# Performance work log

Hardware: AMD Instinct MI355X
Metric: run time of the kernel (lower is better)

Reference implementation:

```python
import jax, jax.numpy as jnp
import numpy as np

B, C, H, W = 4, 64, 256, 256
HEADS, DHEAD = 4, 64
INNER = HEADS * DHEAD


def setup_inputs() -> dict:
    key = jax.random.key(0)
    ks = jax.random.split(key, 8)
    s = 1.0 / np.sqrt(C)
    return {
        "x_in": jax.random.normal(ks[0], (B, C, H, W), jnp.float32),
        "illu_fea_trans": jax.random.normal(ks[1], (B, C, H, W), jnp.float32),
        "Wq": jax.random.normal(ks[2], (C, INNER), jnp.float32) * s,
        "Wk": jax.random.normal(ks[3], (C, INNER), jnp.float32) * s,
        "Wv": jax.random.normal(ks[4], (C, INNER), jnp.float32) * s,
        "WL": jax.random.normal(ks[5], (C, INNER), jnp.float32) * s,
        "rescale": jnp.ones((HEADS, 1, 1), jnp.float32),
        "Wp": jax.random.normal(ks[6], (INNER, C), jnp.float32) / np.sqrt(INNER),
        "bp": jnp.zeros((C,), jnp.float32),
    }


def _l2norm(t, axis=-1, eps=1e-12):
    # matches torch F.normalize(p=2): x / max(||x||, eps)
    n = jnp.sqrt(jnp.sum(t * t, axis=axis, keepdims=True))
    return t / jnp.maximum(n, eps)


def reference(x_in, illu_fea_trans, Wq, Wk, Wv, WL, rescale, Wp, bp):
    b, c, h, w = x_in.shape
    n = h * w
    # NCHW -> [b, n, c]
    x = jnp.transpose(x_in, (0, 2, 3, 1)).reshape(b, n, c)
    illu = jnp.transpose(illu_fea_trans, (0, 2, 3, 1)).reshape(b, n, c)

    def split_heads(t):  # [b,n,inner] -> [b,heads,d,n] (transposed attention)
        return jnp.transpose(t.reshape(b, n, HEADS, DHEAD), (0, 2, 3, 1))

    q = split_heads(x @ Wq)           # [b,h,d,n]
    k = split_heads(x @ Wk)
    v = split_heads(x @ Wv) * split_heads(illu @ WL)  # illumination-gated v

    q = _l2norm(q, axis=-1)
    k = _l2norm(k, axis=-1)
    attn = jnp.einsum('bhdn,bhen->bhde', k, q)  # [b,h,d,d]
    attn = jax.nn.softmax(attn * rescale[None], axis=-1)
    out = jnp.einsum('bhde,bhen->bhdn', attn, v)  # [b,h,d,n]

    # [b,h,d,n] -> [b,n,inner]
    out = jnp.transpose(out, (0, 3, 1, 2)).reshape(b, n, INNER)
    out = out @ Wp + bp  # [b,n,c]
    return jnp.transpose(out.reshape(b, h, w, c), (0, 3, 1, 2))  # [b,c,h,w]
```

## Files before the change

### kernel.cpp

```cpp
#include <hip/hip_runtime.h>
#include <hip/hip_bf16.h>


#define NPOS 65536
#define CH 64
#define INNER 256

typedef __attribute__((ext_vector_type(8))) __bf16 bfrag;
typedef __attribute__((ext_vector_type(4))) float facc;
typedef __attribute__((ext_vector_type(4))) float fvec4;

__device__ __forceinline__ unsigned short f2bu(float f) {
  return __builtin_bit_cast(unsigned short, (__bf16)f);
}

#define SWA(row, colbyte) ((row) * 128 + ((colbyte) ^ (((row) & 7) << 4)))

__global__ __launch_bounds__(256) void k1_xx(const float* __restrict__ x,
                                             float* __restrict__ xx) {
  const int b = blockIdx.y;
  const int wave = threadIdx.x >> 6, lane = threadIdx.x & 63;
  const int r = lane & 15, g = lane >> 4;
  const int gw = blockIdx.x * 4 + wave;
  const int per = NPOS / 128;
  const size_t n0 = (size_t)gw * per;
  const float* xb = x + (size_t)b * CH * NPOS;

  facc acc[4][4] = {};

  for (int n = 0; n < per; n += 32) {
    bfrag fr[4];
#pragma unroll
    for (int t = 0; t < 4; ++t) {
      const float* p = xb + (size_t)(16 * t + r) * NPOS + n0 + n + g * 8;
      fvec4 lo = *(const fvec4*)p;
      fvec4 hi = *(const fvec4*)(p + 4);
      bfrag f;
#pragma unroll
      for (int e = 0; e < 4; ++e) { f[e] = (__bf16)lo[e]; f[e + 4] = (__bf16)hi[e]; }
      fr[t] = f;
    }
#pragma unroll
    for (int ti = 0; ti < 4; ++ti)
#pragma unroll
      for (int tj = 0; tj < 4; ++tj)
        acc[ti][tj] = __builtin_amdgcn_mfma_f32_16x16x32_bf16(fr[ti], fr[tj],
                                                              acc[ti][tj], 0, 0, 0);
  }

  __shared__ float red[4][4096];
  float* my = red[wave];
#pragma unroll
  for (int ti = 0; ti < 4; ++ti)
#pragma unroll
    for (int tj = 0; tj < 4; ++tj)
#pragma unroll
      for (int q = 0; q < 4; ++q)
        my[(16 * ti + g * 4 + q) * 64 + 16 * tj + r] = acc[ti][tj][q];
  __syncthreads();
  float* xxb = xx + (size_t)b * 4096;
  for (int i = threadIdx.x; i < 4096; i += 256)
    atomicAdd(xxb + i, red[0][i] + red[1][i] + red[2][i] + red[3][i]);
}

__global__ __launch_bounds__(256) void k2_attn(
    const float* __restrict__ xx, const float* __restrict__ Wq,
    const float* __restrict__ Wk, const float* __restrict__ rescale,
    const float* __restrict__ Wp, unsigned short* __restrict__ Mt) {
  const int b = blockIdx.x >> 2, h = blockIdx.x & 3;
  const int t = threadIdx.x;
  const int wave = t >> 6, lane = t & 63;
  const int r = lane & 15, g = lane >> 4;

  __shared__ __align__(16) char tXX[8192];
  __shared__ __align__(16) char tWq[8192];
  __shared__ __align__(16) char tWk[8192];
  __shared__ __align__(16) char tWp[8192];
  __shared__ __align__(16) char tZq[8192];
  __shared__ __align__(16) char tZk[8192];
  __shared__ __align__(16) char tAt[8192];
  __shared__ float gG[64][68];
  __shared__ float sMx[64][4], sSm[64][4];
  __shared__ float sNq[64], sNk[64];

  const float* xxb = xx + (size_t)b * 4096;
#pragma unroll
  for (int rep = 0; rep < 16; ++rep) {
    int idx = rep * 256 + t;
    int row = idx >> 6, col = idx & 63;
    *(unsigned short*)(tXX + SWA(row, col * 2)) = f2bu(xxb[idx]);
    float vq = Wq[row * INNER + h * 64 + col];
    float vk = Wk[row * INNER + h * 64 + col];
    *(unsigned short*)(tWq + SWA(col, row * 2)) = f2bu(vq);
    *(unsigned short*)(tWk + SWA(col, row * 2)) = f2bu(vk);
    *(unsigned short*)(tWp + SWA(col, row * 2)) = f2bu(Wp[(h * 64 + row) * CH + col]);
  }
  __syncthreads();

  facc zq[4] = {}, zk[4] = {};
#pragma unroll
  for (int s = 0; s < 2; ++s) {
    bfrag aq = *(const bfrag*)(tWq + SWA(16 * wave + r, s * 64 + g * 16));
    bfrag ak = *(const bfrag*)(tWk + SWA(16 * wave + r, s * 64 + g * 16));
#pragma unroll
    for (int tj = 0; tj < 4; ++tj) {
      bfrag bx = *(const bfrag*)(tXX + SWA(16 * tj + r, s * 64 + g * 16));
      zq[tj] = __builtin_amdgcn_mfma_f32_16x16x32_bf16(aq, bx, zq[tj], 0, 0, 0);
      zk[tj] = __builtin_amdgcn_mfma_f32_16x16x32_bf16(ak, bx, zk[tj], 0, 0, 0);
    }
  }
#pragma unroll
  for (int tj = 0; tj < 4; ++tj)
#pragma unroll
    for (int q = 0; q < 4; ++q) {
      int row = 16 * wave + g * 4 + q, colb = (16 * tj + r) * 2;
      *(unsigned short*)(tZq + SWA(row, colb)) = f2bu(zq[tj][q]);
      *(unsigned short*)(tZk + SWA(row, colb)) = f2bu(zk[tj][q]);
    }
  __syncthreads();

  facc ga[4] = {}, q2[4] = {}, k2[4] = {};
#pragma unroll
  for (int s = 0; s < 2; ++s) {
    bfrag azk = *(const bfrag*)(tZk + SWA(16 * wave + r, s * 64 + g * 16));
    bfrag azq = *(const bfrag*)(tZq + SWA(16 * wave + r, s * 64 + g * 16));
#pragma unroll
    for (int tj = 0; tj < 4; ++tj) {
      bfrag bq = *(const bfrag*)(tWq + SWA(16 * tj + r, s * 64 + g * 16));
      bfrag bk = *(const bfrag*)(tWk + SWA(16 * tj + r, s * 64 + g * 16));
      ga[tj] = __builtin_amdgcn_mfma_f32_16x16x32_bf16(azk, bq, ga[tj], 0, 0, 0);
      q2[tj] = __builtin_amdgcn_mfma_f32_16x16x32_bf16(azq, bq, q2[tj], 0, 0, 0);
      k2[tj] = __builtin_amdgcn_mfma_f32_16x16x32_bf16(azk, bk, k2[tj], 0, 0, 0);
    }
  }
#pragma unroll
  for (int tj = 0; tj < 4; ++tj)
#pragma unroll
    for (int q = 0; q < 4; ++q) {
      int row = 16 * wave + g * 4 + q, col = 16 * tj + r;
      gG[row][col] = ga[tj][q];
      if (row == col) { sNq[row] = q2[tj][q]; sNk[row] = k2[tj][q]; }
    }
  __syncthreads();

  if (t < 64) {
    sNq[t] = 1.f / fmaxf(sqrtf(sNq[t]), 1e-12f);
    sNk[t] = rescale[h] / fmaxf(sqrtf(sNk[t]), 1e-12f);
  }
  __syncthreads();

  {
    const int d = t >> 2, p = t & 3;
    const float ik = sNk[d];
    float le[16];
    float mx = -1e30f;
#pragma unroll
    for (int j = 0; j < 16; ++j) {
      float v = gG[d][16 * p + j] * ik * sNq[16 * p + j];
      le[j] = v; mx = fmaxf(mx, v);
    }
    sMx[d][p] = mx;
    __syncthreads();
    mx = fmaxf(fmaxf(sMx[d][0], sMx[d][1]), fmaxf(sMx[d][2], sMx[d][3]));
    float sm = 0.f;
#pragma unroll
    for (int j = 0; j < 16; ++j) { le[j] = __expf(le[j] - mx); sm += le[j]; }
    sSm[d][p] = sm;
    __syncthreads();
    sm = sSm[d][0] + sSm[d][1] + sSm[d][2] + sSm[d][3];
    const float inv = 1.f / sm;
#pragma unroll
    for (int j = 0; j < 16; ++j) {
      int e = 16 * p + j;
      *(unsigned short*)(tAt + SWA(e, d * 2)) = f2bu(le[j] * inv);
    }
  }
  __syncthreads();

  facc m[4] = {};
#pragma unroll
  for (int s = 0; s < 2; ++s) {
    bfrag aa = *(const bfrag*)(tAt + SWA(16 * wave + r, s * 64 + g * 16));
#pragma unroll
    for (int tj = 0; tj < 4; ++tj) {
      bfrag bw = *(const bfrag*)(tWp + SWA(16 * tj + r, s * 64 + g * 16));
      m[tj] = __builtin_amdgcn_mfma_f32_16x16x32_bf16(aa, bw, m[tj], 0, 0, 0);
    }
  }
#pragma unroll
  for (int tj = 0; tj < 4; ++tj)
#pragma unroll
    for (int q = 0; q < 4; ++q) {
      int e = 16 * wave + g * 4 + q, c2 = 16 * tj + r;
      Mt[((size_t)(b * CH + c2)) * INNER + h * 64 + e] = f2bu(m[tj][q]);
    }
}

__global__ __launch_bounds__(256) void k3_out(
    const float* __restrict__ x, const float* __restrict__ illu,
    const float* __restrict__ Wv, const float* __restrict__ WL,
    const unsigned short* __restrict__ Mt, const float* __restrict__ bp,
    float* __restrict__ out) {
  const int b = blockIdx.y;
  const int wave = threadIdx.x >> 6, lane = threadIdx.x & 63;
  const int r = lane & 15, g = lane >> 4;
  const int BJ = 512;
  const int n0 = blockIdx.x * BJ;

  __shared__ char lxs[2][8192];
  __shared__ char lis[2][8192];
  __shared__ char lvs[2][8192];

  bfrag wvA[4][2], wlA[4][2], mtA[8];
#pragma unroll
  for (int ti = 0; ti < 4; ++ti) {
#pragma unroll
    for (int s = 0; s < 2; ++s) {
      bfrag fv, fl;
      const int i = wave * 64 + ti * 16 + r;
#pragma unroll
      for (int e = 0; e < 8; ++e) {
        const int c = 32 * s + g * 8 + e;
        fv[e] = (__bf16)Wv[c * INNER + i];
        fl[e] = (__bf16)WL[c * INNER + i];
      }
      wvA[ti][s] = fv; wlA[ti][s] = fl;
    }
  }
#pragma unroll
  for (int s8 = 0; s8 < 8; ++s8)
    mtA[s8] = *(const bfrag*)(Mt + ((size_t)(b * CH + wave * 16 + r)) * INNER + s8 * 32 + g * 8);
  float bcol[4];
#pragma unroll
  for (int q = 0; q < 4; ++q) bcol[q] = bp[wave * 16 + g * 4 + q];

  const float* xb = x + (size_t)b * CH * NPOS;
  const float* ib = illu + (size_t)b * CH * NPOS;
  float* ob = out + (size_t)b * CH * NPOS;

  const int sc2 = threadIdx.x >> 3;
  const int sjo = (threadIdx.x & 7) * 8;

  for (int chunk = 0; chunk < BJ / 64; ++chunk) {
    const int cb = chunk & 1;
    const int nbase = n0 + chunk * 64;
    {
      const float* px0 = xb + (size_t)(2 * sc2) * NPOS + nbase + sjo;
      const float* pi0 = ib + (size_t)(2 * sc2) * NPOS + nbase + sjo;
      fvec4 xa0 = *(const fvec4*)px0,         xa1 = *(const fvec4*)(px0 + 4);
      fvec4 xb0 = *(const fvec4*)(px0 + NPOS), xb1 = *(const fvec4*)(px0 + NPOS + 4);
      fvec4 ia0 = *(const fvec4*)pi0,         ia1 = *(const fvec4*)(pi0 + 4);
      fvec4 ib0 = *(const fvec4*)(pi0 + NPOS), ib1 = *(const fvec4*)(pi0 + NPOS + 4);
#pragma unroll
      for (int jj = 0; jj < 8; ++jj) {
        const int j = sjo + jj;
        const int byte = (sc2 * 4) ^ ((j & 7) << 4);
        float x0 = jj < 4 ? xa0[jj & 3] : xa1[jj & 3];
        float x1 = jj < 4 ? xb0[jj & 3] : xb1[jj & 3];
        float i0 = jj < 4 ? ia0[jj & 3] : ia1[jj & 3];
        float i1 = jj < 4 ? ib0[jj & 3] : ib1[jj & 3];
        *(unsigned int*)(lxs[cb] + j * 128 + byte) =
            (unsigned int)f2bu(x0) | ((unsigned int)f2bu(x1) << 16);
        *(unsigned int*)(lis[cb] + j * 128 + byte) =
            (unsigned int)f2bu(i0) | ((unsigned int)f2bu(i1) << 16);
      }
    }
    __syncthreads();

#pragma unroll
    for (int sub = 0; sub < 4; ++sub) {
      const int vb = sub & 1;
      const int j0 = sub * 16;
      const int j = j0 + r;
      bfrag xB[2], iB[2];
#pragma unroll
      for (int s = 0; s < 2; ++s) {
        const int byte = (s * 64 + g * 16) ^ ((j & 7) << 4);
        xB[s] = *(const bfrag*)(lxs[cb] + j * 128 + byte);
        iB[s] = *(const bfrag*)(lis[cb] + j * 128 + byte);
      }
      facc av[4] = {}, gv[4] = {};
#pragma unroll
      for (int ti = 0; ti < 4; ++ti) {
#pragma unroll
        for (int s = 0; s < 2; ++s) {
          av[ti] = __builtin_amdgcn_mfma_f32_16x16x32_bf16(wvA[ti][s], xB[s], av[ti], 0, 0, 0);
          gv[ti] = __builtin_amdgcn_mfma_f32_16x16x32_bf16(wlA[ti][s], iB[s], gv[ti], 0, 0, 0);
        }
      }
#pragma unroll
      for (int ti = 0; ti < 4; ++ti) {
        const float v0 = av[ti][0] * gv[ti][0], v1 = av[ti][1] * gv[ti][1];
        const float v2 = av[ti][2] * gv[ti][2], v3 = av[ti][3] * gv[ti][3];
        const int i = wave * 64 + ti * 16 + g * 4;
        const int sw = (r & 7) << 4;
        *(unsigned int*)(lvs[vb] + r * 512 + ((i * 2) ^ sw)) =
            (unsigned int)f2bu(v0) | ((unsigned int)f2bu(v1) << 16);
        *(unsigned int*)(lvs[vb] + r * 512 + (((i + 2) * 2) ^ sw)) =
            (unsigned int)f2bu(v2) | ((unsigned int)f2bu(v3) << 16);
      }
      __syncthreads();
      facc ov = {0.f, 0.f, 0.f, 0.f};
#pragma unroll
      for (int s8 = 0; s8 < 8; ++s8) {
        const int byte = (s8 * 64 + g * 16) ^ ((r & 7) << 4);
        bfrag vB = *(const bfrag*)(lvs[vb] + r * 512 + byte);
        ov = __builtin_amdgcn_mfma_f32_16x16x32_bf16(mtA[s8], vB, ov, 0, 0, 0);
      }
#pragma unroll
      for (int q = 0; q < 4; ++q)
        ob[(size_t)(wave * 16 + g * 4 + q) * NPOS + nbase + j0 + r] = ov[q] + bcol[q];
      __syncthreads();
    }
  }
}

extern "C" void kernel_launch(void* const* d_in, const int* in_sizes, int n_in,
                              void* d_out, int out_size, void* d_ws, size_t ws_size,
                              hipStream_t stream) {
  (void)in_sizes; (void)n_in; (void)out_size; (void)ws_size;
  const float* x    = (const float*)d_in[0];
  const float* illu = (const float*)d_in[1];
  const float* Wq   = (const float*)d_in[2];
  const float* Wk   = (const float*)d_in[3];
  const float* Wv   = (const float*)d_in[4];
  const float* WL   = (const float*)d_in[5];
  const float* rsc  = (const float*)d_in[6];
  const float* Wp   = (const float*)d_in[7];
  const float* bp   = (const float*)d_in[8];
  float* out = (float*)d_out;

  float* xxws = (float*)d_ws;
  unsigned short* Mt = (unsigned short*)((char*)d_ws + 4 * 4096 * sizeof(float));

  hipMemsetAsync(d_ws, 0, (size_t)4 * 4096 * sizeof(float), stream);
  hipLaunchKernelGGL(k1_xx, dim3(32, 4), dim3(256), 0, stream, x, xxws);
  hipLaunchKernelGGL(k2_attn, dim3(16), dim3(256), 0, stream, xxws, Wq, Wk, rsc, Wp, Mt);
  hipLaunchKernelGGL(k3_out, dim3(128, 4), dim3(256), 0, stream, x, illu, Wv, WL, Mt, bp, out);
}
```

Measured before the change: 82.45 us.

## Pre-transpose bf16 V/L weights, shrink k3 tiles, and refine LDS swizzle and syncs

Adds a small kernel that converts Wv and WL to bf16 and transposes them once, so k3 can load each weight fragment with one vector read instead of 16 strided scalar fp32 loads per fragment. k3 now handles 256 positions per block, doubling the grid to 1024 blocks. The x/illu LDS staging is single-buffered. The swizzle now mixes higher row bits to cut bank conflicts, and the trailing per-sub __syncthreads is removed because the v buffer is still double-buffered. The cost is an extra kernel launch and more per-block prologue work (loading weights and Mt) spread over more, smaller blocks.

```diff
diff --git a/kernel.cpp b/kernel.cpp
--- a/kernel.cpp
+++ b/kernel.cpp
@@ -15,6 +15,16 @@
 }
 
 #define SWA(row, colbyte) ((row) * 128 + ((colbyte) ^ (((row) & 7) << 4)))
+
+__global__ __launch_bounds__(256) void k0_wt(const float* __restrict__ Wv,
+                                             const float* __restrict__ WL,
+                                             unsigned short* __restrict__ WvT,
+                                             unsigned short* __restrict__ WLT) {
+  int t = blockIdx.x * 256 + threadIdx.x;
+  int c = t >> 8, i = t & 255;
+  WvT[i * CH + c] = f2bu(Wv[c * INNER + i]);
+  WLT[i * CH + c] = f2bu(WL[c * INNER + i]);
+}
 
 __global__ __launch_bounds__(256) void k1_xx(const float* __restrict__ x,
                                              float* __restrict__ xx) {
@@ -198,33 +208,26 @@
 
 __global__ __launch_bounds__(256) void k3_out(
     const float* __restrict__ x, const float* __restrict__ illu,
-    const float* __restrict__ Wv, const float* __restrict__ WL,
+    const unsigned short* __restrict__ WvT, const unsigned short* __restrict__ WLT,
     const unsigned short* __restrict__ Mt, const float* __restrict__ bp,
     float* __restrict__ out) {
   const int b = blockIdx.y;
   const int wave = threadIdx.x >> 6, lane = threadIdx.x & 63;
   const int r = lane & 15, g = lane >> 4;
-  const int BJ = 512;
-  const int n0 = blockIdx.x * BJ;
-
-  __shared__ char lxs[2][8192];
-  __shared__ char lis[2][8192];
-  __shared__ char lvs[2][8192];
+  const int n0 = blockIdx.x * 256;
+
+  __shared__ __align__(16) char lxs[8192];
+  __shared__ __align__(16) char lis[8192];
+  __shared__ __align__(16) char lvs[2][8192];
 
   bfrag wvA[4][2], wlA[4][2], mtA[8];
 #pragma unroll
   for (int ti = 0; ti < 4; ++ti) {
+    const int i = wave * 64 + ti * 16 + r;
 #pragma unroll
     for (int s = 0; s < 2; ++s) {
-      bfrag fv, fl;
-      const int i = wave * 64 + ti * 16 + r;
-#pragma unroll
-      for (int e = 0; e < 8; ++e) {
-        const int c = 32 * s + g * 8 + e;
-        fv[e] = (__bf16)Wv[c * INNER + i];
-        fl[e] = (__bf16)WL[c * INNER + i];
-      }
-      wvA[ti][s] = fv; wlA[ti][s] = fl;
+      wvA[ti][s] = *(const bfrag*)(WvT + i * CH + s * 32 + g * 8);
+      wlA[ti][s] = *(const bfrag*)(WLT + i * CH + s * 32 + g * 8);
     }
   }
 #pragma unroll
@@ -241,27 +244,26 @@
   const int sc2 = threadIdx.x >> 3;
   const int sjo = (threadIdx.x & 7) * 8;
 
-  for (int chunk = 0; chunk < BJ / 64; ++chunk) {
-    const int cb = chunk & 1;
+  for (int chunk = 0; chunk < 4; ++chunk) {
     const int nbase = n0 + chunk * 64;
     {
       const float* px0 = xb + (size_t)(2 * sc2) * NPOS + nbase + sjo;
       const float* pi0 = ib + (size_t)(2 * sc2) * NPOS + nbase + sjo;
-      fvec4 xa0 = *(const fvec4*)px0,         xa1 = *(const fvec4*)(px0 + 4);
+      fvec4 xa0 = *(const fvec4*)px0,          xa1 = *(const fvec4*)(px0 + 4);
       fvec4 xb0 = *(const fvec4*)(px0 + NPOS), xb1 = *(const fvec4*)(px0 + NPOS + 4);
-      fvec4 ia0 = *(const fvec4*)pi0,         ia1 = *(const fvec4*)(pi0 + 4);
+      fvec4 ia0 = *(const fvec4*)pi0,          ia1 = *(const fvec4*)(pi0 + 4);
       fvec4 ib0 = *(const fvec4*)(pi0 + NPOS), ib1 = *(const fvec4*)(pi0 + NPOS + 4);
 #pragma unroll
       for (int jj = 0; jj < 8; ++jj) {
         const int j = sjo + jj;
-        const int byte = (sc2 * 4) ^ ((j & 7) << 4);
+        const int byte = (sc2 * 4) ^ (((j ^ (j >> 3)) & 7) << 4);
         float x0 = jj < 4 ? xa0[jj & 3] : xa1[jj & 3];
         float x1 = jj < 4 ? xb0[jj & 3] : xb1[jj & 3];
         float i0 = jj < 4 ? ia0[jj & 3] : ia1[jj & 3];
         float i1 = jj < 4 ? ib0[jj & 3] : ib1[jj & 3];
-        *(unsigned int*)(lxs[cb] + j * 128 + byte) =
+        *(unsigned int*)(lxs + j * 128 + byte) =
             (unsigned int)f2bu(x0) | ((unsigned int)f2bu(x1) << 16);
-        *(unsigned int*)(lis[cb] + j * 128 + byte) =
+        *(unsigned int*)(lis + j * 128 + byte) =
             (unsigned int)f2bu(i0) | ((unsigned int)f2bu(i1) << 16);
       }
     }
@@ -272,12 +274,13 @@
       const int vb = sub & 1;
       const int j0 = sub * 16;
       const int j = j0 + r;
+      const int swv = ((j ^ (j >> 3)) & 7) << 4;
       bfrag xB[2], iB[2];
 #pragma unroll
       for (int s = 0; s < 2; ++s) {
-        const int byte = (s * 64 + g * 16) ^ ((j & 7) << 4);
-        xB[s] = *(const bfrag*)(lxs[cb] + j * 128 + byte);
-        iB[s] = *(const bfrag*)(lis[cb] + j * 128 + byte);
+        const int byte = (s * 64 + g * 16) ^ swv;
+        xB[s] = *(const bfrag*)(lxs + j * 128 + byte);
+        iB[s] = *(const bfrag*)(lis + j * 128 + byte);
       }
       facc av[4] = {}, gv[4] = {};
 #pragma unroll
@@ -310,7 +313,6 @@
 #pragma unroll
       for (int q = 0; q < 4; ++q)
         ob[(size_t)(wave * 16 + g * 4 + q) * NPOS + nbase + j0 + r] = ov[q] + bcol[q];
-      __syncthreads();
     }
   }
 }
@@ -331,10 +333,13 @@
   float* out = (float*)d_out;
 
   float* xxws = (float*)d_ws;
-  unsigned short* Mt = (unsigned short*)((char*)d_ws + 4 * 4096 * sizeof(float));
+  unsigned short* Mt  = (unsigned short*)((char*)d_ws + 65536);
+  unsigned short* WvT = (unsigned short*)((char*)d_ws + 65536 + 131072);
+  unsigned short* WLT = WvT + INNER * CH;
 
   hipMemsetAsync(d_ws, 0, (size_t)4 * 4096 * sizeof(float), stream);
+  hipLaunchKernelGGL(k0_wt, dim3(64), dim3(256), 0, stream, Wv, WL, WvT, WLT);
   hipLaunchKernelGGL(k1_xx, dim3(32, 4), dim3(256), 0, stream, x, xxws);
   hipLaunchKernelGGL(k2_attn, dim3(16), dim3(256), 0, stream, xxws, Wq, Wk, rsc, Wp, Mt);
-  hipLaunchKernelGGL(k3_out, dim3(128, 4), dim3(256), 0, stream, x, illu, Wv, WL, Mt, bp, out);
-}
+  hipLaunchKernelGGL(k3_out, dim3(256, 4), dim3(256), 0, stream, x, illu, WvT, WLT, Mt, bp, out);
+}
```

New measurement: 83.96 us. About the same (+1.8%).
